# Kernel optimization log

Hardware: AMD Instinct MI355X
Metric: run time of the kernel (lower is better)

Reference implementation:

```python
import jax, jax.numpy as jnp
import numpy as np


def _conv(x, w, b, pad):
    # x: (B,C,H,W), w: (O,I,kh,kw), NCHW conv with given padding
    y = jax.lax.conv_general_dilated(x, w, window_strides=(1, 1), padding=pad,
                                     dimension_numbers=('NCHW', 'OIHW', 'NCHW'))
    return y + b[None, :, None, None]


def _frn(x, eps):
    # FilterResponseNorm: normalize by rms over spatial dims (2,3)
    nu2 = jnp.mean(x * x, axis=(2, 3), keepdims=True)
    return x * jax.lax.rsqrt(nu2 + jnp.abs(eps))


def _mish(x):
    return x * jnp.tanh(jax.nn.softplus(x))


def setup_inputs() -> dict:
    key = jax.random.key(0)
    ks = jax.random.split(key, 9)
    B, C, H, W = 4, 256, 64, 64
    C16 = C // 16
    x = jax.random.normal(ks[0], (B, C, H, W), dtype=jnp.float32)
    s = 0.05
    wq = jax.random.normal(ks[1], (C16, C, 1, 3), dtype=jnp.float32) * s
    bq = jax.random.normal(ks[2], (C16,), dtype=jnp.float32) * s
    wk = jax.random.normal(ks[3], (C16, C, 3, 1), dtype=jnp.float32) * s
    bk = jax.random.normal(ks[4], (C16,), dtype=jnp.float32) * s
    wv = jax.random.normal(ks[5], (C, C, 1, 1), dtype=jnp.float32) * s
    bv = jax.random.normal(ks[6], (C,), dtype=jnp.float32) * s
    gamma = jax.random.normal(ks[7], (1,), dtype=jnp.float32) * 0.1
    eps_q = jnp.full((1, C16, 1, 1), 1e-6, dtype=jnp.float32)
    eps_k = jnp.full((1, C16, 1, 1), 1e-6, dtype=jnp.float32)
    return {"x": x, "wq": wq, "bq": bq, "wk": wk, "bk": bk,
            "wv": wv, "bv": bv, "gamma": gamma, "eps_q": eps_q, "eps_k": eps_k}


def reference(x, wq, bq, wk, bk, wv, bv, gamma, eps_q, eps_k):
    B, C, H, W = x.shape
    N = H * W
    # query branch: Conv2d(k=(1,3), pad=(0,1)) -> FRN -> Mish
    q = _mish(_frn(_conv(x, wq, bq, [(0, 0), (1, 1)]), eps_q))  # (B,C16,H,W)
    # key branch: Conv2d(k=(3,1), pad=(1,0)) -> FRN -> Mish
    k = _mish(_frn(_conv(x, wk, bk, [(1, 1), (0, 0)]), eps_k))  # (B,C16,H,W)
    q = q.reshape(B, -1, N)  # (B,C16,N)
    k = k.reshape(B, -1, N)  # (B,C16,N)
    # affinity[b,n,m] = sum_c q[b,c,n] * k[b,c,m]; softmax over m
    affinity = jnp.einsum('bcn,bcm->bnm', q, k)
    affinity = jax.nn.softmax(affinity, axis=-1)  # (B,N,N)
    v = _conv(x, wv, bv, [(0, 0), (0, 0)]).reshape(B, C, N)  # (B,C,N)
    # weights = v @ affinity^T : weights[b,c,j] = sum_n v[b,c,n] * affinity[b,j,n]
    weights = jnp.einsum('bcn,bjn->bcj', v, affinity).reshape(B, C, H, W)
    return gamma * weights + x
```

## Files before the change

kernel.cpp:

```cpp
#include <hip/hip_runtime.h>
#include <stdint.h>

#define NB 4
#define CC 256
#define C16 16
#define HH 64
#define WW 64
#define NN 4096

typedef __attribute__((ext_vector_type(8))) short short8;
typedef __attribute__((ext_vector_type(4))) float floatx4;
typedef __attribute__((ext_vector_type(16))) float floatx16;

#if __has_builtin(__builtin_amdgcn_exp2f)
#define EXP2(x) __builtin_amdgcn_exp2f(x)
#else
#define EXP2(x) exp2f(x)
#endif

__device__ __forceinline__ unsigned short f2bf(float f) {
    union { float f; unsigned u; } v; v.f = f;
    unsigned r = v.u + 0x7fffu + ((v.u >> 16) & 1u);
    return (unsigned short)(r >> 16);
}
__device__ __forceinline__ float bf2f(unsigned short h) {
    union { unsigned u; float f; } v; v.u = (unsigned)h << 16;
    return v.f;
}



__device__ __forceinline__ void prep_tile_body(
        int vb, const float* __restrict__ x, unsigned short* __restrict__ xT,
        float (*tile_t)[65], int tid) {
    int nt = vb & 63, ct = (vb >> 6) & 3, b = vb >> 8;
    int n0 = nt * 64, c0 = ct * 64;
    int rg = tid >> 4, f = tid & 15;
    const float* xb = x + ((size_t)b * CC + c0) * NN + n0;
#pragma unroll
    for (int p = 0; p < 4; ++p) {
        int c = p * 16 + rg;
        float4 v = *(const float4*)(xb + (size_t)c * NN + f * 4);
        tile_t[f * 4 + 0][c] = v.x;
        tile_t[f * 4 + 1][c] = v.y;
        tile_t[f * 4 + 2][c] = v.z;
        tile_t[f * 4 + 3][c] = v.w;
    }
    __syncthreads();
    unsigned short* xtb = xT + (((size_t)b * 8 + ct * 2 + (f >> 3)) * NN + n0) * 32 + (f & 7) * 4;
#pragma unroll
    for (int p = 0; p < 4; ++p) {
        int n = p * 16 + rg;
        ushort4 st;
        st.x = f2bf(tile_t[n][f * 4 + 0]);
        st.y = f2bf(tile_t[n][f * 4 + 1]);
        st.z = f2bf(tile_t[n][f * 4 + 2]);
        st.w = f2bf(tile_t[n][f * 4 + 3]);
        *(ushort4*)(xtb + (size_t)n * 32) = st;
    }
}

__device__ __forceinline__ void prep_wt_body(
        int vb, const float* __restrict__ wv, const float* __restrict__ wq,
        const float* __restrict__ wk, unsigned short* __restrict__ wvb,
        unsigned short* __restrict__ wqkb, float* __restrict__ nu2, int tid) {
    int idx = (vb - 1024) * 256 + tid;
    if (vb == 1024 && tid < 128) nu2[tid] = 0.f;
    if (idx < 16384) {
        float4 v = *(const float4*)(wv + idx * 4);
        ushort4 o;
        o.x = f2bf(v.x); o.y = f2bf(v.y); o.z = f2bf(v.z); o.w = f2bf(v.w);
        int e0 = idx * 4;
        int co = e0 >> 8, c = e0 & 255;
        *(ushort4*)(wvb + ((size_t)(c >> 5) * 256 + co) * 32 + (c & 31)) = o;
    } else if (idx < 16384 + 6144) {
        int base = (idx - 16384) * 4;
#pragma unroll
        for (int u = 0; u < 4; ++u) {
            int e = base + u;
            int t = e / 12288;
            int i = e - t * 12288;
            int tap = i >> 12, o = (i >> 8) & 15, c = i & 255;
            const float* src = t ? wk : wq;
            wqkb[(((size_t)(t * 3 + tap) * 8 + (c >> 5)) * 16 + o) * 32 + (c & 31)]
                = f2bf(src[o * 768 + c * 3 + tap]);
        }
    }
}

__device__ __forceinline__ void conv_v_body(
        int vb, const unsigned short* __restrict__ xT, const unsigned short* __restrict__ wvb,
        const float* __restrict__ bv, unsigned short* __restrict__ vbuf, int tid) {
    int wv_ = tid >> 6, lane = tid & 63;
    int q16 = lane >> 4, c16 = lane & 15;
    int ntile = vb & 63, b = (vb >> 6) & 3, ch = vb >> 8;
    int n0 = ntile * 64;
    int cb = ch * 128 + wv_ * 32;
    floatx4 fzero = {0.f, 0.f, 0.f, 0.f};
    floatx4 acc[2][4];
    for (int ct = 0; ct < 2; ++ct)
        for (int nt = 0; nt < 4; ++nt) acc[ct][nt] = fzero;
    int lo8 = q16 * 8;
    for (int kc = 0; kc < 8; ++kc) {
        const unsigned short* xk = xT + (((size_t)b * 8 + kc) * NN + n0) * 32;
        const unsigned short* wk_ = wvb + ((size_t)kc * 256 + cb) * 32;
        short8 a0 = *(const short8*)(wk_ + c16 * 32 + lo8);
        short8 a1 = *(const short8*)(wk_ + (16 + c16) * 32 + lo8);
        short8 bf[4];
#pragma unroll
        for (int nt = 0; nt < 4; ++nt)
            bf[nt] = *(const short8*)(xk + (nt * 16 + c16) * 32 + lo8);
#pragma unroll
        for (int nt = 0; nt < 4; ++nt) {
            acc[0][nt] = __builtin_amdgcn_mfma_f32_16x16x32_bf16(bf[nt], a0, acc[0][nt], 0, 0, 0);
            acc[1][nt] = __builtin_amdgcn_mfma_f32_16x16x32_bf16(bf[nt], a1, acc[1][nt], 0, 0, 0);
        }
    }
    float bv0 = bv[cb + c16], bv1 = bv[cb + 16 + c16];
    int off = 32 * 8 * (q16 >> 1) + (q16 & 1) * 4 + c16 * 8;
#pragma unroll
    for (int ct = 0; ct < 2; ++ct) {
        float bvv = ct ? bv1 : bv0;
#pragma unroll
        for (int nt = 0; nt < 4; ++nt) {
            size_t fb = (((size_t)b * 8 + ch * 4 + wv_) * 256 + (n0 >> 4) + nt) * 512;
            ushort4 st;
            st.x = f2bf(acc[ct][nt][0] + bvv);
            st.y = f2bf(acc[ct][nt][1] + bvv);
            st.z = f2bf(acc[ct][nt][2] + bvv);
            st.w = f2bf(acc[ct][nt][3] + bvv);
            *(ushort4*)(vbuf + fb + off + ct * 16 * 8) = st;
        }
    }
}

__device__ __forceinline__ void conv_qk_body_v2(
        int u, const unsigned short* __restrict__ xT, const unsigned short* __restrict__ wqkb,
        const float* __restrict__ bq, const float* __restrict__ bk,
        unsigned short* __restrict__ qrawh, unsigned short* __restrict__ krawh,
        float* __restrict__ nu2, int tid,
        float4 (*redq)[64], float4 (*redk)[64]) {
    int w = tid >> 6, lane = tid & 63;
    int q16 = lane >> 4, c16 = lane & 15;
    int b = u >> 8, unit = u & 255;
    int n0 = unit * 16;
    int nl = n0 + c16;
    int hh = nl >> 6, ww = nl & 63;
    bool vm1 = (ww != 0), vp1 = (ww != 63);
    bool vm64 = (hh != 0), vp64 = (hh != 63);
    short8 zero8 = {0, 0, 0, 0, 0, 0, 0, 0};
    floatx4 accq = {0.f, 0.f, 0.f, 0.f}, acck = {0.f, 0.f, 0.f, 0.f};
    int lo8 = q16 * 8;
#pragma unroll
    for (int kk = 0; kk < 2; ++kk) {
        int kc = w * 2 + kk;
        const unsigned short* xk = xT + (((size_t)b * 8 + kc) * NN) * 32;
        short8 b0 = *(const short8*)(xk + (size_t)nl * 32 + lo8);
        short8 bm1 = vm1 ? *(const short8*)(xk + (size_t)(nl - 1) * 32 + lo8) : zero8;
        short8 bp1 = vp1 ? *(const short8*)(xk + (size_t)(nl + 1) * 32 + lo8) : zero8;
        short8 bm64 = vm64 ? *(const short8*)(xk + (size_t)(nl - 64) * 32 + lo8) : zero8;
        short8 bp64 = vp64 ? *(const short8*)(xk + (size_t)(nl + 64) * 32 + lo8) : zero8;
        int wbase = kc * 512 + c16 * 32 + lo8;
        short8 aq0 = *(const short8*)(wqkb + 0 * 4096 + wbase);
        short8 aq1 = *(const short8*)(wqkb + 1 * 4096 + wbase);
        short8 aq2 = *(const short8*)(wqkb + 2 * 4096 + wbase);
        short8 ak0 = *(const short8*)(wqkb + 12288 + 0 * 4096 + wbase);
        short8 ak1 = *(const short8*)(wqkb + 12288 + 1 * 4096 + wbase);
        short8 ak2 = *(const short8*)(wqkb + 12288 + 2 * 4096 + wbase);
        accq = __builtin_amdgcn_mfma_f32_16x16x32_bf16(bm1, aq0, accq, 0, 0, 0);
        accq = __builtin_amdgcn_mfma_f32_16x16x32_bf16(b0, aq1, accq, 0, 0, 0);
        accq = __builtin_amdgcn_mfma_f32_16x16x32_bf16(bp1, aq2, accq, 0, 0, 0);
        acck = __builtin_amdgcn_mfma_f32_16x16x32_bf16(bm64, ak0, acck, 0, 0, 0);
        acck = __builtin_amdgcn_mfma_f32_16x16x32_bf16(b0, ak1, acck, 0, 0, 0);
        acck = __builtin_amdgcn_mfma_f32_16x16x32_bf16(bp64, ak2, acck, 0, 0, 0);
    }
    float4 pq, pk;
    pq.x = accq[0]; pq.y = accq[1]; pq.z = accq[2]; pq.w = accq[3];
    pk.x = acck[0]; pk.y = acck[1]; pk.z = acck[2]; pk.w = acck[3];
    redq[w][lane] = pq;
    redk[w][lane] = pk;
    __syncthreads();
    if (w == 0) {
        float4 a0 = redq[0][lane], a1 = redq[1][lane], a2 = redq[2][lane], a3 = redq[3][lane];
        float s0 = ((a0.x + a1.x) + a2.x) + a3.x;
        float s1 = ((a0.y + a1.y) + a2.y) + a3.y;
        float s2 = ((a0.z + a1.z) + a2.z) + a3.z;
        float s3 = ((a0.w + a1.w) + a2.w) + a3.w;
        float bqv = bq[c16];
        float vq0 = s0 + bqv, vq1 = s1 + bqv, vq2 = s2 + bqv, vq3 = s3 + bqv;
        ushort4 sq4;
        sq4.x = f2bf(vq0); sq4.y = f2bf(vq1); sq4.z = f2bf(vq2); sq4.w = f2bf(vq3);
        *(ushort4*)(qrawh + (size_t)(b * C16 + c16) * NN + n0 + q16 * 4) = sq4;
        float ssq = vq0 * vq0 + vq1 * vq1 + vq2 * vq2 + vq3 * vq3;
        ssq += __shfl_xor(ssq, 16, 64);
        ssq += __shfl_xor(ssq, 32, 64);
        if (lane < 16) atomicAdd(nu2 + b * C16 + lane, ssq);
    } else if (w == 1) {
        float4 a0 = redk[0][lane], a1 = redk[1][lane], a2 = redk[2][lane], a3 = redk[3][lane];
        float s0 = ((a0.x + a1.x) + a2.x) + a3.x;
        float s1 = ((a0.y + a1.y) + a2.y) + a3.y;
        float s2 = ((a0.z + a1.z) + a2.z) + a3.z;
        float s3 = ((a0.w + a1.w) + a2.w) + a3.w;
        float bkv = bk[c16];
        float vk0 = s0 + bkv, vk1 = s1 + bkv, vk2 = s2 + bkv, vk3 = s3 + bkv;
        ushort4 sk4;
        sk4.x = f2bf(vk0); sk4.y = f2bf(vk1); sk4.z = f2bf(vk2); sk4.w = f2bf(vk3);
        *(ushort4*)(krawh + (size_t)(b * C16 + c16) * NN + n0 + q16 * 4) = sk4;
        float ssk = vk0 * vk0 + vk1 * vk1 + vk2 * vk2 + vk3 * vk3;
        ssk += __shfl_xor(ssk, 16, 64);
        ssk += __shfl_xor(ssk, 32, 64);
        if (lane < 16) atomicAdd(nu2 + 64 + b * C16 + lane, ssk);
    }
}

__device__ __forceinline__ void frn_body(
        int blk, const unsigned short* __restrict__ qrawh, const unsigned short* __restrict__ krawh,
        const float* __restrict__ nu2, const float* __restrict__ eps_q,
        const float* __restrict__ eps_k, unsigned short* __restrict__ qb,
        unsigned short* __restrict__ kb, int tid) {
    int tensor = blk >> 8;
    int b = (blk >> 6) & 3;
    int nch = blk & 63;
    const unsigned short* raw = tensor ? krawh : qrawh;
    const float* eps = tensor ? eps_k : eps_q;
    unsigned short* outp = tensor ? kb : qb;
    const float* nu = nu2 + tensor * 64 + b * C16;
    float scale = tensor ? 1.0f : 1.44269504f;
    int n = nch * 64 + (tid & 63);
    int oq = tid >> 6;
    ushort4 pk4;
#pragma unroll
    for (int i = 0; i < 4; ++i) {
        int o = oq * 4 + i;
        float r = bf2f(raw[(size_t)(b * C16 + o) * NN + n]);
        float v = r * rsqrtf(nu[o] * (1.f / (float)NN) + fabsf(eps[o]));
        float t = EXP2(v * 1.44269504f);
        float num = t * t + 2.0f * t;
        float m = (v * num) * __builtin_amdgcn_rcpf(num + 2.0f);
        if (v > 30.f) m = v;
        m *= scale;
        ((unsigned short*)&pk4)[i] = f2bf(m);
    }
    size_t base = ((size_t)b * 128 + (n >> 5)) * 512 + (size_t)(n & 31) * 8
                + (size_t)(oq >> 1) * 256 + (oq & 1) * 4;
    *(ushort4*)(outp + base) = pk4;
}

__device__ __forceinline__ void pack_half(
        const floatx16& sc, int h, short8* A, float* lsum) {
    unsigned pk[4];
    float ls = 0.f;
#pragma unroll
    for (int p = 0; p < 4; ++p) {
        float e0 = EXP2(sc[8 * h + 2 * p]);
        float e1 = EXP2(sc[8 * h + 2 * p + 1]);
        ls += e0 + e1;
        pk[p] = __builtin_amdgcn_perm(__float_as_uint(e1), __float_as_uint(e0), 0x07060302u);
    }
    *lsum += ls;
    asm("v_permlane32_swap_b32 %0, %1" : "+v"(pk[0]), "+v"(pk[2]));
    asm("v_permlane32_swap_b32 %0, %1" : "+v"(pk[1]), "+v"(pk[3]));
    union { unsigned u[4]; short8 s; } a;
    a.u[0] = pk[0]; a.u[1] = pk[1]; a.u[2] = pk[2]; a.u[3] = pk[3];
    *A = a.s;
}

__device__ __forceinline__ void attn_body(
        int id, const unsigned short* __restrict__ qb, const unsigned short* __restrict__ kb,
        const unsigned short* __restrict__ vbuf, const float* __restrict__ x,
        const float* __restrict__ gamma_p, float* __restrict__ out,
        float (*lpart)[2][32], float (*obuf)[32][33], int tid) {
    int wv_ = __builtin_amdgcn_readfirstlane(tid >> 6);
    int lane = tid & 63;
    int l31 = lane & 31, lh = lane >> 5;
    int cs = id & 1, b = (id >> 1) & 3, jt = id >> 3;
    int jbase = jt * 64, cb = cs * 128;
    int lane8 = lane * 8;

    const unsigned short* qfb = qb + ((size_t)b * 128 + (jbase >> 5)) * 512 + lane8;
    const unsigned short* kfb = kb + ((size_t)b * 128 + (wv_ * 32)) * 512 + lane8;

    short8 qf0 = *(const short8*)qfb;
    short8 qf1 = *(const short8*)(qfb + 512);

    floatx16 z16 = {0,0,0,0,0,0,0,0,0,0,0,0,0,0,0,0};
    floatx16 acc0[4], acc1[4];
#pragma unroll
    for (int cg = 0; cg < 4; ++cg) { acc0[cg] = z16; acc1[cg] = z16; }
    float lsum0 = 0.f, lsum1 = 0.f;

    const unsigned short* vp0 = vbuf + (((size_t)b * 8 + cs * 4 + 0) * 256 + wv_ * 64) * 512 + lane8;
    const unsigned short* vp1 = vbuf + (((size_t)b * 8 + cs * 4 + 1) * 256 + wv_ * 64) * 512 + lane8;
    const unsigned short* vp2 = vbuf + (((size_t)b * 8 + cs * 4 + 2) * 256 + wv_ * 64) * 512 + lane8;
    const unsigned short* vp3 = vbuf + (((size_t)b * 8 + cs * 4 + 3) * 256 + wv_ * 64) * 512 + lane8;

    short8 ak = *(const short8*)kfb;
#pragma unroll 1
    for (int step = 0; step < 32; ++step) {
        short8 vf0a = *(const short8*)vp0;
        short8 vf1a = *(const short8*)vp1;
        short8 vf2a = *(const short8*)vp2;
        short8 vf3a = *(const short8*)vp3;
        short8 vf0b = *(const short8*)(vp0 + 512);
        short8 vf1b = *(const short8*)(vp1 + 512);
        short8 vf2b = *(const short8*)(vp2 + 512);
        short8 vf3b = *(const short8*)(vp3 + 512);
        floatx16 sc0 = __builtin_amdgcn_mfma_f32_32x32x16_bf16(ak, qf0, z16, 0, 0, 0);
        floatx16 sc1 = __builtin_amdgcn_mfma_f32_32x32x16_bf16(ak, qf1, z16, 0, 0, 0);
        ak = *(const short8*)(kfb + (size_t)((step + 1) & 31) * 512);
        short8 A;
        pack_half(sc0, 0, &A, &lsum0);
        __builtin_amdgcn_s_setprio(1);
        acc0[0] = __builtin_amdgcn_mfma_f32_32x32x16_bf16(A, vf0a, acc0[0], 0, 0, 0);
        acc0[1] = __builtin_amdgcn_mfma_f32_32x32x16_bf16(A, vf1a, acc0[1], 0, 0, 0);
        acc0[2] = __builtin_amdgcn_mfma_f32_32x32x16_bf16(A, vf2a, acc0[2], 0, 0, 0);
        acc0[3] = __builtin_amdgcn_mfma_f32_32x32x16_bf16(A, vf3a, acc0[3], 0, 0, 0);
        __builtin_amdgcn_s_setprio(0);
        __builtin_amdgcn_sched_barrier(0);
        pack_half(sc0, 1, &A, &lsum0);
        __builtin_amdgcn_s_setprio(1);
        acc0[0] = __builtin_amdgcn_mfma_f32_32x32x16_bf16(A, vf0b, acc0[0], 0, 0, 0);
        acc0[1] = __builtin_amdgcn_mfma_f32_32x32x16_bf16(A, vf1b, acc0[1], 0, 0, 0);
        acc0[2] = __builtin_amdgcn_mfma_f32_32x32x16_bf16(A, vf2b, acc0[2], 0, 0, 0);
        acc0[3] = __builtin_amdgcn_mfma_f32_32x32x16_bf16(A, vf3b, acc0[3], 0, 0, 0);
        __builtin_amdgcn_s_setprio(0);
        __builtin_amdgcn_sched_barrier(0);
        pack_half(sc1, 0, &A, &lsum1);
        __builtin_amdgcn_s_setprio(1);
        acc1[0] = __builtin_amdgcn_mfma_f32_32x32x16_bf16(A, vf0a, acc1[0], 0, 0, 0);
        acc1[1] = __builtin_amdgcn_mfma_f32_32x32x16_bf16(A, vf1a, acc1[1], 0, 0, 0);
        acc1[2] = __builtin_amdgcn_mfma_f32_32x32x16_bf16(A, vf2a, acc1[2], 0, 0, 0);
        acc1[3] = __builtin_amdgcn_mfma_f32_32x32x16_bf16(A, vf3a, acc1[3], 0, 0, 0);
        __builtin_amdgcn_s_setprio(0);
        __builtin_amdgcn_sched_barrier(0);
        pack_half(sc1, 1, &A, &lsum1);
        __builtin_amdgcn_s_setprio(1);
        acc1[0] = __builtin_amdgcn_mfma_f32_32x32x16_bf16(A, vf0b, acc1[0], 0, 0, 0);
        acc1[1] = __builtin_amdgcn_mfma_f32_32x32x16_bf16(A, vf1b, acc1[1], 0, 0, 0);
        acc1[2] = __builtin_amdgcn_mfma_f32_32x32x16_bf16(A, vf2b, acc1[2], 0, 0, 0);
        acc1[3] = __builtin_amdgcn_mfma_f32_32x32x16_bf16(A, vf3b, acc1[3], 0, 0, 0);
        __builtin_amdgcn_s_setprio(0);
        vp0 += 1024; vp1 += 1024; vp2 += 1024; vp3 += 1024;
    }

    lsum0 += __shfl_xor(lsum0, 32, 64);
    lsum1 += __shfl_xor(lsum1, 32, 64);
    if (lh == 0) { lpart[wv_][0][l31] = lsum0; lpart[wv_][1][l31] = lsum1; }
    __syncthreads();

    int j31 = tid & 31;
    float gamma = gamma_p[0];
    float gl0 = gamma / (lpart[0][0][j31] + lpart[1][0][j31] + lpart[2][0][j31] + lpart[3][0][j31]);
    float gl1 = gamma / (lpart[0][1][j31] + lpart[1][1][j31] + lpart[2][1][j31] + lpart[3][1][j31]);
    const float* xbb = x + (size_t)b * CC * NN;
    float* obb = out + (size_t)b * CC * NN;
    int hofs = lh * 4;
    int cgrp = tid >> 5;
#pragma unroll
    for (int jg = 0; jg < 2; ++jg) {
        float gl = jg ? gl1 : gl0;
#pragma unroll
        for (int cg = 0; cg < 4; ++cg) {
            __syncthreads();
            const floatx16& a = jg ? acc1[cg] : acc0[cg];
#pragma unroll
            for (int r = 0; r < 16; ++r) {
                int row = (r & 3) + 8 * (r >> 2) + hofs;
                obuf[wv_][row][l31] = a[r];
            }
            __syncthreads();
#pragma unroll
            for (int i = 0; i < 4; ++i) {
                int c = cgrp * 4 + i;
                float val = obuf[0][j31][c] + obuf[1][j31][c] + obuf[2][j31][c] + obuf[3][j31][c];
                size_t oidx = (size_t)(cb + cg * 32 + c) * NN + jbase + jg * 32 + j31;
                obb[oidx] = fmaf(gl, val, xbb[oidx]);
            }
        }
    }
}

__global__ __launch_bounds__(256) void prep_kernel(
        const float* __restrict__ x, const float* __restrict__ wv,
        const float* __restrict__ wq, const float* __restrict__ wk,
        unsigned short* __restrict__ xT, unsigned short* __restrict__ wvb,
        unsigned short* __restrict__ wqkb, float* __restrict__ nu2) {
    __shared__ float tile_t[64][65];
    int bid = blockIdx.x;
    if (bid < 1024) prep_tile_body(bid, x, xT, tile_t, threadIdx.x);
    else prep_wt_body(bid, wv, wq, wk, wvb, wqkb, nu2, threadIdx.x);
}

__global__ __launch_bounds__(256) void conv_kernel(
        const unsigned short* __restrict__ xT, const unsigned short* __restrict__ wvb,
        const unsigned short* __restrict__ wqkb, const float* __restrict__ bv,
        const float* __restrict__ bq, const float* __restrict__ bk,
        unsigned short* __restrict__ vbuf, unsigned short* __restrict__ qrawh,
        unsigned short* __restrict__ krawh, float* __restrict__ nu2) {
    __shared__ float4 redq[4][64];
    __shared__ float4 redk[4][64];
    int bid = blockIdx.x;
    if (bid < 512) conv_v_body(bid, xT, wvb, bv, vbuf, threadIdx.x);
    else conv_qk_body_v2(bid - 512, xT, wqkb, bq, bk, qrawh, krawh, nu2,
                         threadIdx.x, redq, redk);
}

__global__ __launch_bounds__(256) void frn_mish_kernel(
        const unsigned short* __restrict__ qrawh, const unsigned short* __restrict__ krawh,
        const float* __restrict__ nu2, const float* __restrict__ eps_q,
        const float* __restrict__ eps_k, unsigned short* __restrict__ qb,
        unsigned short* __restrict__ kb) {
    frn_body(blockIdx.x, qrawh, krawh, nu2, eps_q, eps_k, qb, kb, threadIdx.x);
}

__global__ __launch_bounds__(256, 2) void attn_kernel(
        const unsigned short* __restrict__ qb, const unsigned short* __restrict__ kb,
        const unsigned short* __restrict__ vbuf, const float* __restrict__ x,
        const float* __restrict__ gamma_p, float* __restrict__ out) {
    __shared__ float lpart[4][2][32];
    __shared__ float obuf[4][32][33];
    attn_body(blockIdx.x, qb, kb, vbuf, x, gamma_p, out, lpart, obuf, threadIdx.x);
}

extern "C" void kernel_launch(void* const* d_in, const int* in_sizes, int n_in,
                              void* d_out, int out_size, void* d_ws, size_t ws_size,
                              hipStream_t stream) {
    const float* x     = (const float*)d_in[0];
    const float* wq    = (const float*)d_in[1];
    const float* bq    = (const float*)d_in[2];
    const float* wk    = (const float*)d_in[3];
    const float* bk    = (const float*)d_in[4];
    const float* wv    = (const float*)d_in[5];
    const float* bv    = (const float*)d_in[6];
    const float* gamma = (const float*)d_in[7];
    const float* eps_q = (const float*)d_in[8];
    const float* eps_k = (const float*)d_in[9];
    float* out = (float*)d_out;
    char* ws = (char*)d_ws;

    unsigned short* qrawh = (unsigned short*)ws;
    unsigned short* krawh = (unsigned short*)(ws + (1u << 20));
    float* nu2  = (float*)(ws + (2u << 20));
    unsigned short* qb = (unsigned short*)(ws + (2u << 20) + 4096);
    unsigned short* kb = qb + (size_t)NB * NN * C16;
    unsigned short* vbuf = kb + (size_t)NB * NN * C16;
    unsigned short* xT = vbuf + (size_t)NB * CC * NN;
    unsigned short* wvb = xT + (size_t)NB * NN * CC;
    unsigned short* wqkb = wvb + (size_t)CC * CC;

    prep_kernel<<<dim3(1112), dim3(256), 0, stream>>>(x, wv, wq, wk, xT, wvb, wqkb, nu2);
    conv_kernel<<<dim3(1536), dim3(256), 0, stream>>>(xT, wvb, wqkb, bv, bq, bk, vbuf, qrawh, krawh, nu2);
    frn_mish_kernel<<<dim3(512), dim3(256), 0, stream>>>(qrawh, krawh, nu2, eps_q, eps_k, qb, kb);
    attn_kernel<<<dim3(512), dim3(256), 0, stream>>>(qb, kb, vbuf, x, gamma, out);
}
```

Measured before the change: 151.7 us.

## Fuse FRN+Mish into conv kernel via last-block-per-batch atomic counter

Removes the separate FRN/Mish kernel launch. Each qk conv block increments a per-batch counter after its sum-of-squares atomics. The last block for each batch then applies FRN normalisation and Mish to that batch's q and k. The counters are zeroed in the prep kernel. This saves a launch and an inter-kernel gap, but it serialises the FRN work for each batch onto a single block at the tail of the conv kernel.

```diff
diff --git a/kernel.cpp b/kernel.cpp
--- a/kernel.cpp
+++ b/kernel.cpp
@@ -65,7 +65,10 @@
         const float* __restrict__ wk, unsigned short* __restrict__ wvb,
         unsigned short* __restrict__ wqkb, float* __restrict__ nu2, int tid) {
     int idx = (vb - 1024) * 256 + tid;
-    if (vb == 1024 && tid < 128) nu2[tid] = 0.f;
+    if (vb == 1024) {
+        if (tid < 128) nu2[tid] = 0.f;
+        else if (tid < 132) ((int*)((char*)nu2 + 1024))[tid - 128] = 0;
+    }
     if (idx < 16384) {
         float4 v = *(const float4*)(wv + idx * 4);
         ushort4 o;
@@ -134,12 +137,61 @@
     }
 }
 
+__device__ __forceinline__ void frn_body(
+        int blk, const unsigned short* __restrict__ qrawh, const unsigned short* __restrict__ krawh,
+        const float* __restrict__ nu2, const float* __restrict__ eps_q,
+        const float* __restrict__ eps_k, unsigned short* __restrict__ qb,
+        unsigned short* __restrict__ kb, int tid) {
+    int tensor = blk >> 8;
+    int b = (blk >> 6) & 3;
+    int nch = blk & 63;
+    const unsigned short* raw = tensor ? krawh : qrawh;
+    const float* eps = tensor ? eps_k : eps_q;
+    unsigned short* outp = tensor ? kb : qb;
+    const float* nu = nu2 + tensor * 64 + b * C16;
+    float scale = tensor ? 1.0f : 1.44269504f;
+    int n = nch * 64 + (tid & 63);
+    int oq = tid >> 6;
+    ushort4 pk4;
+#pragma unroll
+    for (int i = 0; i < 4; ++i) {
+        int o = oq * 4 + i;
+        float r = bf2f(raw[(size_t)(b * C16 + o) * NN + n]);
+        float v = r * rsqrtf(nu[o] * (1.f / (float)NN) + fabsf(eps[o]));
+        float t = EXP2(v * 1.44269504f);
+        float num = t * t + 2.0f * t;
+        float m = (v * num) * __builtin_amdgcn_rcpf(num + 2.0f);
+        if (v > 30.f) m = v;
+        m *= scale;
+        ((unsigned short*)&pk4)[i] = f2bf(m);
+    }
+    size_t base = ((size_t)b * 128 + (n >> 5)) * 512 + (size_t)(n & 31) * 8
+                + (size_t)(oq >> 1) * 256 + (oq & 1) * 4;
+    *(ushort4*)(outp + base) = pk4;
+}
+
+__device__ __forceinline__ void frn_for_b(
+        int b, const unsigned short* __restrict__ qrawh, const unsigned short* __restrict__ krawh,
+        const float* __restrict__ nu2, const float* __restrict__ eps_q,
+        const float* __restrict__ eps_k, unsigned short* __restrict__ qb,
+        unsigned short* __restrict__ kb, int tid) {
+#pragma unroll 4
+    for (int seg = 0; seg < 128; ++seg) {
+        int tensor = seg >> 6;
+        int nch = seg & 63;
+        frn_body((tensor << 8) | (b << 6) | nch, qrawh, krawh, nu2, eps_q, eps_k,
+                 qb, kb, tid);
+    }
+}
+
 __device__ __forceinline__ void conv_qk_body_v2(
         int u, const unsigned short* __restrict__ xT, const unsigned short* __restrict__ wqkb,
         const float* __restrict__ bq, const float* __restrict__ bk,
         unsigned short* __restrict__ qrawh, unsigned short* __restrict__ krawh,
-        float* __restrict__ nu2, int tid,
-        float4 (*redq)[64], float4 (*redk)[64]) {
+        float* __restrict__ nu2, const float* __restrict__ eps_q,
+        const float* __restrict__ eps_k, unsigned short* __restrict__ qb,
+        unsigned short* __restrict__ kb, int tid,
+        float4 (*redq)[64], float4 (*redk)[64], int* lastflag) {
     int w = tid >> 6, lane = tid & 63;
     int q16 = lane >> 4, c16 = lane & 15;
     int b = u >> 8, unit = u & 255;
@@ -211,39 +263,18 @@
         ssk += __shfl_xor(ssk, 32, 64);
         if (lane < 16) atomicAdd(nu2 + 64 + b * C16 + lane, ssk);
     }
-}
-
-__device__ __forceinline__ void frn_body(
-        int blk, const unsigned short* __restrict__ qrawh, const unsigned short* __restrict__ krawh,
-        const float* __restrict__ nu2, const float* __restrict__ eps_q,
-        const float* __restrict__ eps_k, unsigned short* __restrict__ qb,
-        unsigned short* __restrict__ kb, int tid) {
-    int tensor = blk >> 8;
-    int b = (blk >> 6) & 3;
-    int nch = blk & 63;
-    const unsigned short* raw = tensor ? krawh : qrawh;
-    const float* eps = tensor ? eps_k : eps_q;
-    unsigned short* outp = tensor ? kb : qb;
-    const float* nu = nu2 + tensor * 64 + b * C16;
-    float scale = tensor ? 1.0f : 1.44269504f;
-    int n = nch * 64 + (tid & 63);
-    int oq = tid >> 6;
-    ushort4 pk4;
-#pragma unroll
-    for (int i = 0; i < 4; ++i) {
-        int o = oq * 4 + i;
-        float r = bf2f(raw[(size_t)(b * C16 + o) * NN + n]);
-        float v = r * rsqrtf(nu[o] * (1.f / (float)NN) + fabsf(eps[o]));
-        float t = EXP2(v * 1.44269504f);
-        float num = t * t + 2.0f * t;
-        float m = (v * num) * __builtin_amdgcn_rcpf(num + 2.0f);
-        if (v > 30.f) m = v;
-        m *= scale;
-        ((unsigned short*)&pk4)[i] = f2bf(m);
-    }
-    size_t base = ((size_t)b * 128 + (n >> 5)) * 512 + (size_t)(n & 31) * 8
-                + (size_t)(oq >> 1) * 256 + (oq & 1) * 4;
-    *(ushort4*)(outp + base) = pk4;
+    int* cnt = (int*)((char*)nu2 + 1024);
+    __threadfence();
+    __syncthreads();
+    if (tid == 0) {
+        int old = atomicAdd(cnt + b, 1);
+        *lastflag = (old == 255);
+    }
+    __syncthreads();
+    if (*lastflag) {
+        __threadfence();
+        frn_for_b(b, qrawh, krawh, nu2, eps_q, eps_k, qb, kb, tid);
+    }
 }
 
 __device__ __forceinline__ void pack_half(
@@ -396,21 +427,16 @@
         const unsigned short* __restrict__ wqkb, const float* __restrict__ bv,
         const float* __restrict__ bq, const float* __restrict__ bk,
         unsigned short* __restrict__ vbuf, unsigned short* __restrict__ qrawh,
-        unsigned short* __restrict__ krawh, float* __restrict__ nu2) {
+        unsigned short* __restrict__ krawh, float* __restrict__ nu2,
+        const float* __restrict__ eps_q, const float* __restrict__ eps_k,
+        unsigned short* __restrict__ qb, unsigned short* __restrict__ kb) {
     __shared__ float4 redq[4][64];
     __shared__ float4 redk[4][64];
+    __shared__ int lastflag;
     int bid = blockIdx.x;
     if (bid < 512) conv_v_body(bid, xT, wvb, bv, vbuf, threadIdx.x);
     else conv_qk_body_v2(bid - 512, xT, wqkb, bq, bk, qrawh, krawh, nu2,
-                         threadIdx.x, redq, redk);
-}
-
-__global__ __launch_bounds__(256) void frn_mish_kernel(
-        const unsigned short* __restrict__ qrawh, const unsigned short* __restrict__ krawh,
-        const float* __restrict__ nu2, const float* __restrict__ eps_q,
-        const float* __restrict__ eps_k, unsigned short* __restrict__ qb,
-        unsigned short* __restrict__ kb) {
-    frn_body(blockIdx.x, qrawh, krawh, nu2, eps_q, eps_k, qb, kb, threadIdx.x);
+                         eps_q, eps_k, qb, kb, threadIdx.x, redq, redk, &lastflag);
 }
 
 __global__ __launch_bounds__(256, 2) void attn_kernel(
@@ -449,7 +475,7 @@
     unsigned short* wqkb = wvb + (size_t)CC * CC;
 
     prep_kernel<<<dim3(1112), dim3(256), 0, stream>>>(x, wv, wq, wk, xT, wvb, wqkb, nu2);
-    conv_kernel<<<dim3(1536), dim3(256), 0, stream>>>(xT, wvb, wqkb, bv, bq, bk, vbuf, qrawh, krawh, nu2);
-    frn_mish_kernel<<<dim3(512), dim3(256), 0, stream>>>(qrawh, krawh, nu2, eps_q, eps_k, qb, kb);
+    conv_kernel<<<dim3(1536), dim3(256), 0, stream>>>(xT, wvb, wqkb, bv, bq, bk, vbuf,
+                                                      qrawh, krawh, nu2, eps_q, eps_k, qb, kb);
     attn_kernel<<<dim3(512), dim3(256), 0, stream>>>(qb, kb, vbuf, x, gamma, out);
 }
```

Result: slower. 281.5 us (+85.6%).
